# Optimization experiments

Measured on AMD Instinct MI355X. Metric: run time of the kernel, lower is better.

## Reference

```python
import jax, jax.numpy as jnp
import numpy as np

B, T, D, H, L = 8, 128, 400, 300, 45  # batch, max_length, 2*word_lstm_size, hidden, tag_count


def setup_inputs() -> dict:
    key = jax.random.key(0)
    ks = jax.random.split(key, 10)
    s = 0.05
    return {
        "cont_repr": jax.random.normal(ks[0], (B, T, D), jnp.float32),
        "root": jax.random.normal(ks[1], (1, 1, D), jnp.float32),
        "W1a": jax.random.normal(ks[2], (D, H), jnp.float32) * s,
        "W1b": jax.random.normal(ks[3], (D, H), jnp.float32) * s,
        "b1": jnp.zeros((H,), jnp.float32),
        "Wa": jax.random.normal(ks[4], (H, 1), jnp.float32) * s,
        "ba": jnp.zeros((1,), jnp.float32),
        "Wl": jax.random.normal(ks[5], (H, L), jnp.float32) * s,
        "bl": jnp.zeros((L,), jnp.float32),
        "sentence_lengths": jax.random.randint(ks[6], (B,), 0, T + 1),
        "desired_arcs": jax.random.randint(ks[7], (B, T), 0, T + 1),
        "desired_labels": jax.random.randint(ks[8], (B, T), 0, L),
        "use_desired_arcs": 1,
    }


def reference(cont_repr, root, W1a, W1b, b1, Wa, ba, Wl, bl,
              sentence_lengths, desired_arcs, desired_labels, use_desired_arcs):
    b, t, d = cont_repr.shape
    mask = (jnp.arange(t)[None, :] < sentence_lengths[:, None]).astype(cont_repr.dtype)  # [B,T]
    n_valid = jnp.maximum(mask.sum(), 1.0)

    # Dense(concat(tile_a, tile_b)) == tile_a @ W1a + tile_b @ W1b (exact same math,
    # avoids materializing the [B,T,T+1,2D] concat the TF graph builds).
    a_proj = jnp.einsum('btd,dh->bth', cont_repr, W1a)                     # [B,T,H]
    with_root = jnp.concatenate([jnp.broadcast_to(root, (b, 1, d)), cont_repr], axis=1)  # [B,T+1,D]
    b_proj = jnp.einsum('bsd,dh->bsh', with_root, W1b)                     # [B,T+1,H]
    h = jax.nn.relu(a_proj[:, :, None, :] + b_proj[:, None, :, :] + b1)    # [B,T,T+1,H]

    # UAS: arc scorer (units=1) over T+1 head candidates
    arc_logits = jnp.einsum('btsh,ho->btso', h, Wa)[..., 0] + ba[0]        # [B,T,T+1]
    predicted_arcs = jnp.argmax(arc_logits, axis=-1)                        # [B,T]
    arc_logp = jax.nn.log_softmax(arc_logits, axis=-1)
    arc_ce = -jnp.take_along_axis(arc_logp, desired_arcs[..., None], axis=-1)[..., 0]
    uas_loss = (arc_ce * mask).sum() / n_valid

    # LAS: gather pair repr at selected head, score labels
    sel = desired_arcs if use_desired_arcs else predicted_arcs             # [B,T]
    idx = jnp.broadcast_to(sel[:, :, None, None], (b, t, 1, h.shape[-1]))
    sel_h = jnp.take_along_axis(h, idx, axis=2)[:, :, 0, :]                # [B,T,H]
    lab_logits = jnp.einsum('bth,hl->btl', sel_h, Wl) + bl                 # [B,T,L]
    lab_logp = jax.nn.log_softmax(lab_logits, axis=-1)
    lab_ce = -jnp.take_along_axis(lab_logp, desired_labels[..., None], axis=-1)[..., 0]
    las_loss = (lab_ce * mask).sum() / n_valid

    return (uas_loss + las_loss) / 2
```

## Files before the change

kernel.cpp:

```cpp
#include <hip/hip_runtime.h>
#include <hip/hip_bf16.h>
#include <math.h>

#define BN 8
#define TT 128
#define DD 400
#define HH 300
#define LL 45
#define KH 200

__global__ __launch_bounds__(640) void proj_kernel(
    const float* __restrict__ cont, const float* __restrict__ root,
    const float* __restrict__ W1a, const float* __restrict__ W1b,
    const float* __restrict__ b1,
    const int* __restrict__ slen,
    float* __restrict__ AP, float* __restrict__ BP, float* __restrict__ RP,
    float* __restrict__ accum)
{
    __shared__ float red[320][9];
    const int blk = blockIdx.x;
    const int tid = threadIdx.x;
    const int grp = tid / 320;
    const int h   = tid % 320;
    const int d0  = __builtin_amdgcn_readfirstlane(grp * KH);

    if (blk == 256) {
        if (tid == 0) accum[0] = 0.f;
        float acc = 0.f;
        if (h < HH) {
            const float* wp = W1b + (size_t)d0 * HH + h;
            for (int d = 0; d < KH; ++d)
                acc = fmaf(root[d0 + d], wp[(size_t)d * HH], acc);
        }
        if (grp == 1) red[h][0] = acc;
        __syncthreads();
        if (grp == 0 && h < HH) RP[h] = acc + red[h][0];
        return;
    }

    const bool isA = (blk < 128);
    const int rb   = isA ? blk : blk - 128;
    const int row0 = rb * 8;
    if (isA) {
        const int lenb = slen[row0 >> 7];
        if ((row0 & 127) >= lenb) return;
    }

    const float* W    = isA ? W1a : W1b;
    const float* rows = cont + (size_t)row0 * DD + d0;

    float acc[8];
    #pragma unroll
    for (int r = 0; r < 8; ++r) acc[r] = 0.f;

    if (h < HH) {
        const float* wp = W + (size_t)d0 * HH + h;
        float w[8];
        #pragma unroll
        for (int k = 0; k < 8; ++k) w[k] = wp[(size_t)k * HH];
        for (int dc = 0; dc < KH; dc += 8) {
            float wn[8];
            if (dc + 8 < KH) {
                #pragma unroll
                for (int k = 0; k < 8; ++k) wn[k] = wp[(size_t)(dc + 8 + k) * HH];
            } else {
                #pragma unroll
                for (int k = 0; k < 8; ++k) wn[k] = 0.f;
            }
            #pragma unroll
            for (int r = 0; r < 8; ++r) {
                const float* rp = rows + r * DD + dc;
                #pragma unroll
                for (int k = 0; k < 8; ++k)
                    acc[r] = fmaf(rp[k], w[k], acc[r]);
            }
            #pragma unroll
            for (int k = 0; k < 8; ++k) w[k] = wn[k];
        }
    }

    if (grp == 1) {
        #pragma unroll
        for (int r = 0; r < 8; ++r) red[h][r] = acc[r];
    }
    __syncthreads();
    if (grp == 0 && h < HH) {
        const float bb = isA ? b1[h] : 0.f;
        float* dst = (isA ? AP : BP) + (size_t)row0 * HH + h;
        #pragma unroll
        for (int r = 0; r < 8; ++r)
            dst[(size_t)r * HH] = acc[r] + red[h][r] + bb;
    }
}

__global__ __launch_bounds__(256) void score_kernel(
    const float* __restrict__ AP, const float* __restrict__ BP,
    const float* __restrict__ RP,
    const float* __restrict__ Wa, const float* __restrict__ Wl,
    const float* __restrict__ bl,
    const int* __restrict__ slen, const int* __restrict__ des_arcs,
    const int* __restrict__ des_labels, const int* __restrict__ use_des,
    float* __restrict__ accum)
{
    const int blk = blockIdx.x;
    const int b = blk >> 6, tp = blk & 63;
    const int t0 = tp * 2, t1 = t0 + 1;
    const int len = slen[b];
    if (t0 >= len) return;
    const bool act1 = (t1 < len);

    const int tid = threadIdx.x;
    const int lane = tid & 63, wave = tid >> 6;

    __shared__ float logits[2][132];
    __shared__ float selh[2][HH];
    __shared__ float lablg[2][64];
    __shared__ int   sel_s[2];

    const float* ap0 = AP + (size_t)(b * TT + t0) * HH;
    const float* ap1 = ap0 + HH;

    float apr0[5], apr1[5], war[5];
    #pragma unroll
    for (int i = 0; i < 5; ++i) {
        const int h = lane + 64 * i;
        const bool v = (h < HH);
        apr0[i] = v ? ap0[h] : 0.f;
        apr1[i] = v ? ap1[h] : 0.f;
        war[i]  = v ? Wa[h]  : 0.f;
    }

    for (int s = wave; s < TT + 1; s += 4) {
        const float* bp = (s == 0) ? RP : BP + (size_t)(b * TT + s - 1) * HH;
        float p0 = 0.f, p1 = 0.f;
        #pragma unroll
        for (int i = 0; i < 5; ++i) {
            const int h = lane + 64 * i;
            const float bv = (h < HH) ? bp[h] : 0.f;
            p0 = fmaf(fmaxf(apr0[i] + bv, 0.f), war[i], p0);
            p1 = fmaf(fmaxf(apr1[i] + bv, 0.f), war[i], p1);
        }
        #pragma unroll
        for (int off = 32; off; off >>= 1) {
            p0 += __shfl_xor(p0, off, 64);
            p1 += __shfl_xor(p1, off, 64);
        }
        if (lane == 0) { logits[0][s] = p0; logits[1][s] = p1; }
    }
    __syncthreads();

    if (wave < 2) {
        const int tt = wave ? t1 : t0;
        const float* lg = logits[wave];
        const float v0 = lg[lane];
        const float v1 = lg[64 + lane];
        const float v2 = (lane == 0) ? lg[128] : -INFINITY;
        float m = fmaxf(fmaxf(v0, v1), v2);
        #pragma unroll
        for (int off = 32; off; off >>= 1) m = fmaxf(m, __shfl_xor(m, off, 64));
        float e = __expf(v0 - m) + __expf(v1 - m) + ((lane == 0) ? __expf(v2 - m) : 0.f);
        #pragma unroll
        for (int off = 32; off; off >>= 1) e += __shfl_xor(e, off, 64);
        const float lse = m + __logf(e);

        float bv = v0; int bi = lane;
        if (v1 > bv) { bv = v1; bi = 64 + lane; }
        if (lane == 0 && v2 > bv) { bv = v2; bi = 128; }
        #pragma unroll
        for (int off = 32; off; off >>= 1) {
            const float ov = __shfl_xor(bv, off, 64);
            const int   oi = __shfl_xor(bi, off, 64);
            if (ov > bv || (ov == bv && oi < bi)) { bv = ov; bi = oi; }
        }
        if (lane == 0) {
            const int da = des_arcs[b * TT + tt];
            logits[wave][129] = lse - lg[da];
            sel_s[wave] = use_des[0] ? da : bi;
        }
    }
    __syncthreads();

    for (int j = tid; j < 2 * HH; j += 256) {
        const int w2 = (j < HH) ? 0 : 1;
        const int h  = j - w2 * HH;
        const int s  = sel_s[w2];
        const float* bp = (s == 0) ? RP : BP + (size_t)(b * TT + s - 1) * HH;
        const float* ap = w2 ? ap1 : ap0;
        selh[w2][h] = fmaxf(ap[h] + bp[h], 0.f);
    }
    __syncthreads();

    if (wave < 2 && lane < LL) {
        float a = bl[lane];
        for (int h = 0; h < HH; ++h)
            a = fmaf(selh[wave][h], Wl[h * LL + lane], a);
        lablg[wave][lane] = a;
    }
    __syncthreads();

    if (wave < 2) {
        const int tt = wave ? t1 : t0;
        const float v = (lane < LL) ? lablg[wave][lane] : -INFINITY;
        float m = v;
        #pragma unroll
        for (int off = 32; off; off >>= 1) m = fmaxf(m, __shfl_xor(m, off, 64));
        float e = (lane < LL) ? __expf(v - m) : 0.f;
        #pragma unroll
        for (int off = 32; off; off >>= 1) e += __shfl_xor(e, off, 64);
        const float lse = m + __logf(e);
        if (lane == 0 && (wave == 0 || act1)) {
            const float lab_ce = lse - lablg[wave][des_labels[b * TT + tt]];
            atomicAdd(accum, logits[wave][129] + lab_ce);
        }
    }
}

__global__ void finalize_kernel(const float* __restrict__ accum,
                                const int* __restrict__ slen,
                                float* __restrict__ out)
{
    if (threadIdx.x == 0) {
        int n = 0;
        for (int b = 0; b < BN; ++b) {
            int l = slen[b];
            if (l < 0) l = 0;
            if (l > TT) l = TT;
            n += l;
        }
        float nv = (float)n;
        if (nv < 1.f) nv = 1.f;
        out[0] = accum[0] / (2.f * nv);
    }
}

extern "C" void kernel_launch(void* const* d_in, const int* in_sizes, int n_in,
                              void* d_out, int out_size, void* d_ws, size_t ws_size,
                              hipStream_t stream) {
    const float* cont = (const float*)d_in[0];
    const float* root = (const float*)d_in[1];
    const float* W1a  = (const float*)d_in[2];
    const float* W1b  = (const float*)d_in[3];
    const float* b1   = (const float*)d_in[4];
    const float* Wa   = (const float*)d_in[5];
    const float* Wl   = (const float*)d_in[7];
    const float* bl   = (const float*)d_in[8];
    const int* slen   = (const int*)d_in[9];
    const int* darc   = (const int*)d_in[10];
    const int* dlab   = (const int*)d_in[11];
    const int* used   = (const int*)d_in[12];
    float* out = (float*)d_out;

    float* AP    = (float*)d_ws;
    float* BP    = AP + 1024 * HH;
    float* RP    = BP + 1024 * HH;
    float* accum = RP + 320;

    proj_kernel<<<257, 640, 0, stream>>>(cont, root, W1a, W1b, b1, slen, AP, BP, RP, accum);
    score_kernel<<<512, 256, 0, stream>>>(AP, BP, RP, Wa, Wl, bl, slen, darc, dlab, used, accum);
    finalize_kernel<<<1, 64, 0, stream>>>(accum, slen, out);
}
```

Baseline: 52.60 us.

## Split scoring into arc-logit and softmax/label kernels with per-batch root-prefixed BP

The fused score kernel is split into an arc kernel and a per-token softmax/label kernel. The arc kernel computes arc logits for 4 tokens against a 17-head slice per block, which raises parallelism to 2048 blocks and reuses each head row across more tokens. The second kernel does the arc softmax, selected-head gather, label matmul and CE per token with one wave. The root projection is replicated into a [B,129,H] buffer so head indexing has no branch. This adds a kernel launch and a global round trip for the logits.

```diff
diff --git a/kernel.cpp b/kernel.cpp
--- a/kernel.cpp
+++ b/kernel.cpp
@@ -8,13 +8,15 @@
 #define HH 300
 #define LL 45
 #define KH 200
+#define SS 129
+#define ALG_STRIDE 132
 
 __global__ __launch_bounds__(640) void proj_kernel(
     const float* __restrict__ cont, const float* __restrict__ root,
     const float* __restrict__ W1a, const float* __restrict__ W1b,
     const float* __restrict__ b1,
     const int* __restrict__ slen,
-    float* __restrict__ AP, float* __restrict__ BP, float* __restrict__ RP,
+    float* __restrict__ AP, float* __restrict__ BPX,
     float* __restrict__ accum)
 {
     __shared__ float red[320][9];
@@ -34,7 +36,11 @@
         }
         if (grp == 1) red[h][0] = acc;
         __syncthreads();
-        if (grp == 0 && h < HH) RP[h] = acc + red[h][0];
+        if (grp == 0 && h < HH) {
+            const float v = acc + red[h][0];
+            for (int bb = 0; bb < BN; ++bb)
+                BPX[(size_t)bb * SS * HH + h] = v;
+        }
         return;
     }
 
@@ -85,134 +91,158 @@
     }
     __syncthreads();
     if (grp == 0 && h < HH) {
-        const float bb = isA ? b1[h] : 0.f;
-        float* dst = (isA ? AP : BP) + (size_t)row0 * HH + h;
-        #pragma unroll
-        for (int r = 0; r < 8; ++r)
-            dst[(size_t)r * HH] = acc[r] + red[h][r] + bb;
-    }
-}
-
-__global__ __launch_bounds__(256) void score_kernel(
-    const float* __restrict__ AP, const float* __restrict__ BP,
-    const float* __restrict__ RP,
-    const float* __restrict__ Wa, const float* __restrict__ Wl,
-    const float* __restrict__ bl,
+        if (isA) {
+            const float bb = b1[h];
+            float* dst = AP + (size_t)row0 * HH + h;
+            #pragma unroll
+            for (int r = 0; r < 8; ++r)
+                dst[(size_t)r * HH] = acc[r] + red[h][r] + bb;
+        } else {
+            const int b = row0 >> 7, t = row0 & 127;
+            float* dst = BPX + ((size_t)(b * SS + t + 1)) * HH + h;
+            #pragma unroll
+            for (int r = 0; r < 8; ++r)
+                dst[(size_t)r * HH] = acc[r] + red[h][r];
+        }
+    }
+}
+
+__global__ __launch_bounds__(256) void arc_kernel(
+    const float* __restrict__ AP, const float* __restrict__ BPX,
+    const float* __restrict__ Wa, const int* __restrict__ slen,
+    float* __restrict__ ALG)
+{
+    const int blk = blockIdx.x;
+    const int b  = blk >> 8;
+    const int tg = (blk >> 3) & 31;
+    const int sc = blk & 7;
+    const int t0 = tg * 4;
+    if (t0 >= slen[b]) return;
+
+    const int lane = threadIdx.x & 63;
+    const int wave = threadIdx.x >> 6;
+
+    const float* ap = AP + (size_t)(b * TT + t0) * HH;
+    float apr[4][5], war[5];
+    #pragma unroll
+    for (int i = 0; i < 5; ++i) {
+        const int hh = lane + 64 * i;
+        const bool v = (hh < HH);
+        war[i] = v ? Wa[hh] : 0.f;
+        #pragma unroll
+        for (int r = 0; r < 4; ++r)
+            apr[r][i] = v ? ap[(size_t)r * HH + hh] : 0.f;
+    }
+
+    const int s0 = sc * 17;
+    for (int sl = wave; sl < 17; sl += 4) {
+        const int s = s0 + sl;
+        if (s >= SS) break;
+        const float* bp = BPX + (size_t)(b * SS + s) * HH;
+        float bv[5];
+        #pragma unroll
+        for (int i = 0; i < 5; ++i) {
+            const int hh = lane + 64 * i;
+            bv[i] = (hh < HH) ? bp[hh] : 0.f;
+        }
+        float p0 = 0.f, p1 = 0.f, p2 = 0.f, p3 = 0.f;
+        #pragma unroll
+        for (int i = 0; i < 5; ++i) {
+            p0 = fmaf(fmaxf(apr[0][i] + bv[i], 0.f), war[i], p0);
+            p1 = fmaf(fmaxf(apr[1][i] + bv[i], 0.f), war[i], p1);
+            p2 = fmaf(fmaxf(apr[2][i] + bv[i], 0.f), war[i], p2);
+            p3 = fmaf(fmaxf(apr[3][i] + bv[i], 0.f), war[i], p3);
+        }
+        #pragma unroll
+        for (int off = 32; off; off >>= 1) {
+            p0 += __shfl_xor(p0, off, 64);
+            p1 += __shfl_xor(p1, off, 64);
+            p2 += __shfl_xor(p2, off, 64);
+            p3 += __shfl_xor(p3, off, 64);
+        }
+        if (lane == 0) {
+            float* o = ALG + (size_t)(b * TT + t0) * ALG_STRIDE + s;
+            o[0]              = p0;
+            o[ALG_STRIDE]     = p1;
+            o[2 * ALG_STRIDE] = p2;
+            o[3 * ALG_STRIDE] = p3;
+        }
+    }
+}
+
+__global__ __launch_bounds__(64) void smx_kernel(
+    const float* __restrict__ AP, const float* __restrict__ BPX,
+    const float* __restrict__ Wl, const float* __restrict__ bl,
+    const float* __restrict__ ALG,
     const int* __restrict__ slen, const int* __restrict__ des_arcs,
     const int* __restrict__ des_labels, const int* __restrict__ use_des,
     float* __restrict__ accum)
 {
     const int blk = blockIdx.x;
-    const int b = blk >> 6, tp = blk & 63;
-    const int t0 = tp * 2, t1 = t0 + 1;
-    const int len = slen[b];
-    if (t0 >= len) return;
-    const bool act1 = (t1 < len);
-
-    const int tid = threadIdx.x;
-    const int lane = tid & 63, wave = tid >> 6;
-
-    __shared__ float logits[2][132];
-    __shared__ float selh[2][HH];
-    __shared__ float lablg[2][64];
-    __shared__ int   sel_s[2];
-
-    const float* ap0 = AP + (size_t)(b * TT + t0) * HH;
-    const float* ap1 = ap0 + HH;
-
-    float apr0[5], apr1[5], war[5];
+    const int b = blk >> 7, t = blk & 127;
+    if (t >= slen[b]) return;
+    const int lane = threadIdx.x;
+
+    __shared__ float selh[HH];
+
+    const float* lg = ALG + (size_t)blk * ALG_STRIDE;
+    const float v0 = lg[lane];
+    const float v1 = lg[64 + lane];
+    const float v2 = (lane == 0) ? lg[128] : -INFINITY;
+
+    float m = fmaxf(fmaxf(v0, v1), v2);
+    #pragma unroll
+    for (int off = 32; off; off >>= 1) m = fmaxf(m, __shfl_xor(m, off, 64));
+    float e = __expf(v0 - m) + __expf(v1 - m) + ((lane == 0) ? __expf(v2 - m) : 0.f);
+    #pragma unroll
+    for (int off = 32; off; off >>= 1) e += __shfl_xor(e, off, 64);
+    const float arc_lse = m + __logf(e);
+
+    float bv = v0; int bi = lane;
+    if (v1 > bv) { bv = v1; bi = 64 + lane; }
+    if (lane == 0 && v2 > bv) { bv = v2; bi = 128; }
+    #pragma unroll
+    for (int off = 32; off; off >>= 1) {
+        const float ov = __shfl_xor(bv, off, 64);
+        const int   oi = __shfl_xor(bi, off, 64);
+        if (ov > bv || (ov == bv && oi < bi)) { bv = ov; bi = oi; }
+    }
+
+    const int da = des_arcs[b * TT + t];
+    const float arc_ce = arc_lse - lg[da];
+    const int sel = use_des[0] ? da : bi;
+
+    const float* ap = AP + (size_t)blk * HH;
+    const float* bp = BPX + (size_t)(b * SS + sel) * HH;
     #pragma unroll
     for (int i = 0; i < 5; ++i) {
-        const int h = lane + 64 * i;
-        const bool v = (h < HH);
-        apr0[i] = v ? ap0[h] : 0.f;
-        apr1[i] = v ? ap1[h] : 0.f;
-        war[i]  = v ? Wa[h]  : 0.f;
-    }
-
-    for (int s = wave; s < TT + 1; s += 4) {
-        const float* bp = (s == 0) ? RP : BP + (size_t)(b * TT + s - 1) * HH;
-        float p0 = 0.f, p1 = 0.f;
-        #pragma unroll
-        for (int i = 0; i < 5; ++i) {
-            const int h = lane + 64 * i;
-            const float bv = (h < HH) ? bp[h] : 0.f;
-            p0 = fmaf(fmaxf(apr0[i] + bv, 0.f), war[i], p0);
-            p1 = fmaf(fmaxf(apr1[i] + bv, 0.f), war[i], p1);
-        }
-        #pragma unroll
-        for (int off = 32; off; off >>= 1) {
-            p0 += __shfl_xor(p0, off, 64);
-            p1 += __shfl_xor(p1, off, 64);
-        }
-        if (lane == 0) { logits[0][s] = p0; logits[1][s] = p1; }
+        const int hh = lane + 64 * i;
+        if (hh < HH) selh[hh] = fmaxf(ap[hh] + bp[hh], 0.f);
     }
     __syncthreads();
 
-    if (wave < 2) {
-        const int tt = wave ? t1 : t0;
-        const float* lg = logits[wave];
-        const float v0 = lg[lane];
-        const float v1 = lg[64 + lane];
-        const float v2 = (lane == 0) ? lg[128] : -INFINITY;
-        float m = fmaxf(fmaxf(v0, v1), v2);
-        #pragma unroll
-        for (int off = 32; off; off >>= 1) m = fmaxf(m, __shfl_xor(m, off, 64));
-        float e = __expf(v0 - m) + __expf(v1 - m) + ((lane == 0) ? __expf(v2 - m) : 0.f);
-        #pragma unroll
-        for (int off = 32; off; off >>= 1) e += __shfl_xor(e, off, 64);
-        const float lse = m + __logf(e);
-
-        float bv = v0; int bi = lane;
-        if (v1 > bv) { bv = v1; bi = 64 + lane; }
-        if (lane == 0 && v2 > bv) { bv = v2; bi = 128; }
-        #pragma unroll
-        for (int off = 32; off; off >>= 1) {
-            const float ov = __shfl_xor(bv, off, 64);
-            const int   oi = __shfl_xor(bi, off, 64);
-            if (ov > bv || (ov == bv && oi < bi)) { bv = ov; bi = oi; }
-        }
-        if (lane == 0) {
-            const int da = des_arcs[b * TT + tt];
-            logits[wave][129] = lse - lg[da];
-            sel_s[wave] = use_des[0] ? da : bi;
-        }
-    }
-    __syncthreads();
-
-    for (int j = tid; j < 2 * HH; j += 256) {
-        const int w2 = (j < HH) ? 0 : 1;
-        const int h  = j - w2 * HH;
-        const int s  = sel_s[w2];
-        const float* bp = (s == 0) ? RP : BP + (size_t)(b * TT + s - 1) * HH;
-        const float* ap = w2 ? ap1 : ap0;
-        selh[w2][h] = fmaxf(ap[h] + bp[h], 0.f);
-    }
-    __syncthreads();
-
-    if (wave < 2 && lane < LL) {
-        float a = bl[lane];
-        for (int h = 0; h < HH; ++h)
-            a = fmaf(selh[wave][h], Wl[h * LL + lane], a);
-        lablg[wave][lane] = a;
-    }
-    __syncthreads();
-
-    if (wave < 2) {
-        const int tt = wave ? t1 : t0;
-        const float v = (lane < LL) ? lablg[wave][lane] : -INFINITY;
-        float m = v;
-        #pragma unroll
-        for (int off = 32; off; off >>= 1) m = fmaxf(m, __shfl_xor(m, off, 64));
-        float e = (lane < LL) ? __expf(v - m) : 0.f;
-        #pragma unroll
-        for (int off = 32; off; off >>= 1) e += __shfl_xor(e, off, 64);
-        const float lse = m + __logf(e);
-        if (lane == 0 && (wave == 0 || act1)) {
-            const float lab_ce = lse - lablg[wave][des_labels[b * TT + tt]];
-            atomicAdd(accum, logits[wave][129] + lab_ce);
-        }
-    }
+    float a = 0.f;
+    if (lane < LL) {
+        a = bl[lane];
+        for (int hh = 0; hh < HH; hh += 4) {
+            #pragma unroll
+            for (int k = 0; k < 4; ++k)
+                a = fmaf(selh[hh + k], Wl[(hh + k) * LL + lane], a);
+        }
+    }
+    const float v = (lane < LL) ? a : -INFINITY;
+    float lm = v;
+    #pragma unroll
+    for (int off = 32; off; off >>= 1) lm = fmaxf(lm, __shfl_xor(lm, off, 64));
+    float le = (lane < LL) ? __expf(v - lm) : 0.f;
+    #pragma unroll
+    for (int off = 32; off; off >>= 1) le += __shfl_xor(le, off, 64);
+    const float lab_lse = lm + __logf(le);
+
+    const int dl = des_labels[b * TT + t];
+    const float ldl = __shfl(v, dl, 64);
+    if (lane == 0)
+        atomicAdd(accum, arc_ce + (lab_lse - ldl));
 }
 
 __global__ void finalize_kernel(const float* __restrict__ accum,
@@ -251,11 +281,12 @@
     float* out = (float*)d_out;
 
     float* AP    = (float*)d_ws;
-    float* BP    = AP + 1024 * HH;
-    float* RP    = BP + 1024 * HH;
-    float* accum = RP + 320;
-
-    proj_kernel<<<257, 640, 0, stream>>>(cont, root, W1a, W1b, b1, slen, AP, BP, RP, accum);
-    score_kernel<<<512, 256, 0, stream>>>(AP, BP, RP, Wa, Wl, bl, slen, darc, dlab, used, accum);
+    float* BPX   = AP  + 1024 * HH;
+    float* ALG   = BPX + BN * SS * HH;
+    float* accum = ALG + 1024 * ALG_STRIDE;
+
+    proj_kernel<<<257, 640, 0, stream>>>(cont, root, W1a, W1b, b1, slen, AP, BPX, accum);
+    arc_kernel<<<2048, 256, 0, stream>>>(AP, BPX, Wa, slen, ALG);
+    smx_kernel<<<1024, 64, 0, stream>>>(AP, BPX, Wl, bl, ALG, slen, darc, dlab, used, accum);
     finalize_kernel<<<1, 64, 0, stream>>>(accum, slen, out);
 }
```

New measurement: 44.99 us. -14.5%, faster.
